# Kernel tuning notes

Hardware: AMD Instinct MI355X
Metric: run time of the kernel (lower is better)

The kernel has to match this reference:

```python
import jax, jax.numpy as jnp
import numpy as np

EPS = 1e-5  # BatchNorm2d default eps

def setup_inputs() -> dict:
    key = jax.random.key(0)
    k1, k2, k3, k4 = jax.random.split(key, 4)
    B, Cin, Cout, T, V = 64, 64, 128, 300, 25
    x = jax.random.normal(k1, (B, Cin, T, V), dtype=jnp.float32)
    adj = jax.random.uniform(k2, (V, V), dtype=jnp.float32)
    # Conv2d(kernel_size=1) weight (Cout, Cin), kaiming-ish scale
    W = jax.random.normal(k3, (Cout, Cin), dtype=jnp.float32) * (1.0 / np.sqrt(Cin))
    b = jnp.zeros((Cout,), dtype=jnp.float32)
    gamma = jnp.ones((Cout,), dtype=jnp.float32)
    beta = jnp.zeros((Cout,), dtype=jnp.float32)
    return {"x": x, "adj": adj, "W": W, "b": b, "gamma": gamma, "beta": beta}

def reference(x, adj, W, b, gamma, beta):
    # x: (B, C, T, V); graph aggregation over joints: matmul with adj on last dim
    xg = jnp.einsum('bctv,vw->bctw', x, adj)
    # 1x1 conv == per-(t,v) channel projection
    y = jnp.einsum('bctv,oc->botv', xg, W) + b[None, :, None, None]
    # BatchNorm2d (training mode): per-channel stats over (B, T, V), biased var
    mean = jnp.mean(y, axis=(0, 2, 3), keepdims=True)
    var = jnp.mean((y - mean) ** 2, axis=(0, 2, 3), keepdims=True)
    yn = (y - mean) * jax.lax.rsqrt(var + EPS)
    out = jax.nn.relu(gamma[None, :, None, None] * yn + beta[None, :, None, None])
    return out
```

## Files before the change

### kernel.cpp

```cpp
#include <hip/hip_runtime.h>
#include <hip/hip_bf16.h>
#include <stdint.h>

typedef __attribute__((ext_vector_type(8)))  short   short8;
typedef __attribute__((ext_vector_type(16))) float   floatx16;
typedef __attribute__((ext_vector_type(4)))  float   floatx4;

#define B_    64
#define CIN   64
#define COUT  128
#define T_    300
#define V_    25
#define NRED  (B_ * T_ * V_)
#define NSLOTS 32
#define NT    12
#define EPS   1e-5f

__device__ __forceinline__ uint32_t pk2(float a, float b) {
    union { __hip_bfloat162 h; uint32_t u; } c;
    c.h = __float22bfloat162_rn(make_float2(a, b));
    return c.u;
}

__device__ __forceinline__ floatx16 fzero16() {
    floatx16 z;
#pragma unroll
    for (int i = 0; i < 16; ++i) z[i] = 0.f;
    return z;
}

__device__ __forceinline__ int div25(int n) { return (n * 5243) >> 17; }

__device__ __forceinline__ void cvt_hb(const floatx16 h, int q, short8 hb[2]) {
    uint32_t pk[8], pp[8];
#pragma unroll
    for (int i = 0; i < 8; ++i) pk[i] = pk2(h[2 * i], h[2 * i + 1]);
#pragma unroll
    for (int i = 0; i < 8; ++i) pp[i] = (uint32_t)__shfl_xor((int)pk[i], 32, 64);
#pragma unroll
    for (int s = 0; s < 2; ++s) {
        union { short8 sv; uint32_t u[4]; } F;
        F.u[0] = q ? pp[4 * s + 2] : pk[4 * s];
        F.u[1] = q ? pp[4 * s + 3] : pk[4 * s + 1];
        F.u[2] = q ? pk[4 * s + 2] : pp[4 * s];
        F.u[3] = q ? pk[4 * s + 3] : pp[4 * s + 1];
        hb[s] = F.sv;
    }
}

__device__ __forceinline__ void build_const_frags(const float* __restrict__ W,
                                                  const float* __restrict__ adj,
                                                  int wave, int ln, int q,
                                                  short8 wf[4], short8 af[2]) {
    const float* wr = W + (32 * wave + ln) * CIN;
#pragma unroll
    for (int kk = 0; kk < 4; ++kk) {
        int c0 = 16 * kk + 8 * q;
        floatx4 a = *(const floatx4*)(wr + c0);
        floatx4 b = *(const floatx4*)(wr + c0 + 4);
        union { short8 sv; uint32_t u[4]; } F;
        F.u[0] = pk2(a[0], a[1]); F.u[1] = pk2(a[2], a[3]);
        F.u[2] = pk2(b[0], b[1]); F.u[3] = pk2(b[2], b[3]);
        wf[kk] = F.sv;
    }
#pragma unroll
    for (int s = 0; s < 2; ++s) {
        union { short8 sv; uint32_t u[4]; } F;
#pragma unroll
        for (int p = 0; p < 4; ++p) {
            int v0 = 16 * s + 8 * q + 2 * p;
            float e0 = (v0     < V_ && ln < V_) ? adj[v0 * V_ + ln]       : 0.f;
            float e1 = (v0 + 1 < V_ && ln < V_) ? adj[(v0 + 1) * V_ + ln] : 0.f;
            F.u[p] = pk2(e0, e1);
        }
        af[s] = F.sv;
    }
}

__device__ __forceinline__ void stage_x(const float* __restrict__ xb, int t4,
                                        float* __restrict__ ldsx, int tid) {
#pragma unroll
    for (int i = 0; i < 7; ++i) {
        int cid = i * 256 + tid;
        if (i < 6 || tid < 64) {
            int c  = div25(cid);
            int ch = cid - 25 * c;
            *(floatx4*)&ldsx[c * 100 + 4 * ch] =
                *(const floatx4*)(xb + c * 7500 + t4 * 25 + 4 * ch);
        }
    }
}

__device__ __forceinline__ void build_xa_lds(const float* __restrict__ ldsx,
                                             int tloc, int vcl, int q, short8 xa[4]) {
    const float* base = ldsx + tloc * 25 + vcl;
#pragma unroll
    for (int kk = 0; kk < 4; ++kk) {
        union { short8 sv; uint32_t u[4]; } F;
#pragma unroll
        for (int p = 0; p < 4; ++p) {
            int c0 = 16 * kk + 8 * q + 2 * p;
            F.u[p] = pk2(base[c0 * 100], base[(c0 + 1) * 100]);
        }
        xa[kk] = F.sv;
    }
}

__device__ __forceinline__ floatx16 compute_yt(const short8 xa[4], const short8 wf[4],
                                               const short8 af[2], int q) {
    floatx16 h = fzero16();
#pragma unroll
    for (int kk = 0; kk < 4; ++kk)
        h = __builtin_amdgcn_mfma_f32_32x32x16_bf16(xa[kk], wf[kk], h, 0, 0, 0);
    short8 hb[2];
    cvt_hb(h, q, hb);
    floatx16 y = fzero16();
#pragma unroll
    for (int s = 0; s < 2; ++s)
        y = __builtin_amdgcn_mfma_f32_32x32x16_bf16(af[s], hb[s], y, 0, 0, 0);
    return y;
}

__global__ __launch_bounds__(256, 3) void pass1_kernel(
    const float* __restrict__ x, const float* __restrict__ adj,
    const float* __restrict__ W,
    float* __restrict__ psum, float* __restrict__ psq)
{
    __shared__ __attribute__((aligned(16))) float ldsx[6400];

    const int tid  = threadIdx.x;
    const int wave = tid >> 6;
    const int lane = tid & 63;
    const int q    = lane >> 5;
    const int ln   = lane & 31;
    const int b    = blockIdx.y;
    const int tbase = blockIdx.x * NT;

    short8 wf[4], af[2];
    build_const_frags(W, adj, wave, ln, q, wf, af);
    const int vcl = ln < V_ ? ln : V_ - 1;
    const float* xb = x + (size_t)b * (CIN * T_ * V_);

    float sum = 0.f, sq = 0.f;
    for (int g = 0; g < NT / 4; ++g) {
        const int t4 = tbase + 4 * g;
        stage_x(xb, t4, ldsx, tid);
        __syncthreads();
#pragma unroll
        for (int tloc = 0; tloc < 4; ++tloc) {
            short8 xa[4];
            build_xa_lds(ldsx, tloc, vcl, q, xa);
            floatx16 y = compute_yt(xa, wf, af, q);
#pragma unroll
            for (int r = 0; r < 16; ++r) { sum += y[r]; sq += y[r] * y[r]; }
        }
        __syncthreads();
    }

    sum += __shfl_xor(sum, 32, 64);
    sq  += __shfl_xor(sq,  32, 64);
    if (q == 0) {
        int slot = (blockIdx.y * 25 + blockIdx.x) & (NSLOTS - 1);
        atomicAdd(&psum[slot * COUT + 32 * wave + ln], sum);
        atomicAdd(&psq [slot * COUT + 32 * wave + ln], sq);
    }
}

__global__ __launch_bounds__(256, 2) void pass2_kernel(
    const float* __restrict__ x, const float* __restrict__ adj,
    const float* __restrict__ W,
    const float* __restrict__ gamma, const float* __restrict__ beta,
    const float* __restrict__ psum, const float* __restrict__ psq,
    float* __restrict__ out)
{
    __shared__ __attribute__((aligned(16))) float ldsx[6400];
    __shared__ __attribute__((aligned(16))) float ldso[4][3200];

    const int tid  = threadIdx.x;
    const int wave = tid >> 6;
    const int lane = tid & 63;
    const int q    = lane >> 5;
    const int ln   = lane & 31;
    const int b    = blockIdx.y;
    const int tbase = blockIdx.x * NT;
    const int o_l  = 32 * wave + ln;

    short8 wf[4], af[2];
    build_const_frags(W, adj, wave, ln, q, wf, af);

    float s = 0.f, ss = 0.f;
#pragma unroll 4
    for (int k = 0; k < NSLOTS; ++k) {
        s  += psum[k * COUT + o_l];
        ss += psq [k * COUT + o_l];
    }
    const float mean = s / (float)NRED;
    const float var  = ss / (float)NRED - mean * mean;
    const float inv  = rsqrtf(var + EPS);
    const float sc   = gamma[o_l] * inv;
    const float sh   = beta[o_l] - mean * sc;

    const int vcl = ln < V_ ? ln : V_ - 1;
    const float* xb = x + (size_t)b * (CIN * T_ * V_);
    float* const ob = out + (size_t)(b * COUT + 32 * wave) * (T_ * V_);

    for (int g = 0; g < NT / 4; ++g) {
        const int t4 = tbase + 4 * g;
        stage_x(xb, t4, ldsx, tid);
        __syncthreads();

        float* const ow0 = &ldso[wave][ln * 100];
#pragma unroll
        for (int tloc = 0; tloc < 4; ++tloc) {
            short8 xa[4];
            build_xa_lds(ldsx, tloc, vcl, q, xa);
            floatx16 y = compute_yt(xa, wf, af, q);
            float* ow = ow0 + tloc * 25 + 4 * q;
#pragma unroll
            for (int g2 = 0; g2 < 3; ++g2) {
#pragma unroll
                for (int j = 0; j < 4; ++j) {
                    float v = sc * y[4 * g2 + j] + sh;
                    ow[8 * g2 + j] = v > 0.f ? v : 0.f;
                }
            }
            if (q == 0) {
                float v = sc * y[12] + sh;
                ow0[tloc * 25 + 24] = v > 0.f ? v : 0.f;
            }
        }

#pragma unroll
        for (int f = 0; f < 13; ++f) {
            int cid = f * 64 + lane;
            if (f < 12 || lane < 32) {
                int o = div25(cid);
                int c = cid - 25 * o;
                floatx4 v = *(const floatx4*)&ldso[wave][o * 100 + 4 * c];
                *(floatx4*)(ob + (size_t)o * (T_ * V_) + t4 * 25 + 4 * c) = v;
            }
        }
        __syncthreads();
    }
}


extern "C" void kernel_launch(void* const* d_in, const int* in_sizes, int n_in,
                              void* d_out, int out_size, void* d_ws, size_t ws_size,
                              hipStream_t stream) {
    const float* x     = (const float*)d_in[0];
    const float* adj   = (const float*)d_in[1];
    const float* W     = (const float*)d_in[2];
    const float* gamma = (const float*)d_in[4];
    const float* beta  = (const float*)d_in[5];
    float* out = (float*)d_out;

    float* psum = (float*)d_ws;
    float* psq  = (float*)((char*)d_ws + NSLOTS * COUT * sizeof(float));

    hipMemsetAsync(psum, 0, 2 * NSLOTS * COUT * sizeof(float), stream);

    dim3 grid(T_ / NT, B_);
    pass1_kernel<<<grid, 256, 0, stream>>>(x, adj, W, psum, psq);
    pass2_kernel<<<grid, 256, 0, stream>>>(x, adj, W, gamma, beta, psum, psq, out);
}
```

Baseline: 456.9 us.

## Compute transposed output tile and store directly, dropping LDS output staging

Pass 2 now computes the tile with output channels as rows and joints as columns (W-projection MFMA first, then adjacency MFMA), so each lane holds values for one joint across 16 channels. Results are written straight to global memory as scalar stores, removing the 50 KB LDS output buffer and its transpose/copy loop. Per-row BN scale and shift are gathered with lane shuffles, and launch bounds are raised to 3 blocks per SU to use the freed LDS. The trade-off is that the old 16-byte vector stores become scattered 4-byte stores with only 25 contiguous floats per row, and the changed launch bounds may increase register pressure.

```diff
diff --git a/kernel.cpp b/kernel.cpp
--- a/kernel.cpp
+++ b/kernel.cpp
@@ -166,7 +166,7 @@
     }
 }
 
-__global__ __launch_bounds__(256, 2) void pass2_kernel(
+__global__ __launch_bounds__(256, 3) void pass2_kernel(
     const float* __restrict__ x, const float* __restrict__ adj,
     const float* __restrict__ W,
     const float* __restrict__ gamma, const float* __restrict__ beta,
@@ -174,7 +174,6 @@
     float* __restrict__ out)
 {
     __shared__ __attribute__((aligned(16))) float ldsx[6400];
-    __shared__ __attribute__((aligned(16))) float ldso[4][3200];
 
     const int tid  = threadIdx.x;
     const int wave = tid >> 6;
@@ -188,56 +187,56 @@
     short8 wf[4], af[2];
     build_const_frags(W, adj, wave, ln, q, wf, af);
 
-    float s = 0.f, ss = 0.f;
+    float s0 = 0.f, ss = 0.f;
 #pragma unroll 4
     for (int k = 0; k < NSLOTS; ++k) {
-        s  += psum[k * COUT + o_l];
+        s0 += psum[k * COUT + o_l];
         ss += psq [k * COUT + o_l];
     }
-    const float mean = s / (float)NRED;
+    const float mean = s0 / (float)NRED;
     const float var  = ss / (float)NRED - mean * mean;
     const float inv  = rsqrtf(var + EPS);
-    const float sc   = gamma[o_l] * inv;
-    const float sh   = beta[o_l] - mean * sc;
+    const float sc0  = gamma[o_l] * inv;
+    const float sh0  = beta[o_l] - mean * sc0;
+
+    float scr[16], shr[16];
+#pragma unroll
+    for (int r = 0; r < 16; ++r) {
+        int src = (r & 3) + 8 * (r >> 2) + 4 * q;
+        scr[r] = __shfl(sc0, src, 64);
+        shr[r] = __shfl(sh0, src, 64);
+    }
 
     const int vcl = ln < V_ ? ln : V_ - 1;
     const float* xb = x + (size_t)b * (CIN * T_ * V_);
-    float* const ob = out + (size_t)(b * COUT + 32 * wave) * (T_ * V_);
+    float* const ob = out + (size_t)(b * COUT + 32 * wave + 4 * q) * (T_ * V_) + ln;
 
     for (int g = 0; g < NT / 4; ++g) {
         const int t4 = tbase + 4 * g;
         stage_x(xb, t4, ldsx, tid);
         __syncthreads();
-
-        float* const ow0 = &ldso[wave][ln * 100];
 #pragma unroll
         for (int tloc = 0; tloc < 4; ++tloc) {
             short8 xa[4];
             build_xa_lds(ldsx, tloc, vcl, q, xa);
-            floatx16 y = compute_yt(xa, wf, af, q);
-            float* ow = ow0 + tloc * 25 + 4 * q;
-#pragma unroll
-            for (int g2 = 0; g2 < 3; ++g2) {
-#pragma unroll
-                for (int j = 0; j < 4; ++j) {
-                    float v = sc * y[4 * g2 + j] + sh;
-                    ow[8 * g2 + j] = v > 0.f ? v : 0.f;
+            floatx16 h = fzero16();
+#pragma unroll
+            for (int kk = 0; kk < 4; ++kk)
+                h = __builtin_amdgcn_mfma_f32_32x32x16_bf16(xa[kk], wf[kk], h, 0, 0, 0);
+            short8 hb[2];
+            cvt_hb(h, q, hb);
+            floatx16 y = fzero16();
+#pragma unroll
+            for (int s2 = 0; s2 < 2; ++s2)
+                y = __builtin_amdgcn_mfma_f32_32x32x16_bf16(hb[s2], af[s2], y, 0, 0, 0);
+            if (ln < V_) {
+                float* pt = ob + (size_t)(t4 + tloc) * V_;
+#pragma unroll
+                for (int r = 0; r < 16; ++r) {
+                    const int orow = (r & 3) + 8 * (r >> 2);
+                    float v = scr[r] * y[r] + shr[r];
+                    pt[(size_t)orow * (T_ * V_)] = v > 0.f ? v : 0.f;
                 }
-            }
-            if (q == 0) {
-                float v = sc * y[12] + sh;
-                ow0[tloc * 25 + 24] = v > 0.f ? v : 0.f;
-            }
-        }
-
-#pragma unroll
-        for (int f = 0; f < 13; ++f) {
-            int cid = f * 64 + lane;
-            if (f < 12 || lane < 32) {
-                int o = div25(cid);
-                int c = cid - 25 * o;
-                floatx4 v = *(const floatx4*)&ldso[wave][o * 100 + 4 * c];
-                *(floatx4*)(ob + (size_t)o * (T_ * V_) + t4 * 25 + 4 * c) = v;
             }
         }
         __syncthreads();
```

New measurement: 472.1 us. 3.3% more time.

## Stage x tile as XOR-swizzled bf16 transposed layout in LDS

Applied to the files above, without the earlier changes.

The x tile staging now converts pairs of channels to packed bf16 at load time and stores them in a (t,v)-major LDS layout with an XOR swizzle. MFMA A-fragments can then be fetched with a single 128-bit LDS read per k-step instead of eight strided scalar reads plus per-use conversions. This halves the LDS footprint of the x tile and removes the bf16 conversion work repeated across the four waves. The cost is a scattered 32-bit store pattern during staging, and each global load now feeds one channel pair instead of a contiguous float4 row.

```diff
diff --git a/kernel.cpp b/kernel.cpp
--- a/kernel.cpp
+++ b/kernel.cpp
@@ -2,9 +2,10 @@
 #include <hip/hip_bf16.h>
 #include <stdint.h>
 
-typedef __attribute__((ext_vector_type(8)))  short   short8;
-typedef __attribute__((ext_vector_type(16))) float   floatx16;
-typedef __attribute__((ext_vector_type(4)))  float   floatx4;
+typedef __attribute__((ext_vector_type(8)))  short    short8;
+typedef __attribute__((ext_vector_type(16))) float    floatx16;
+typedef __attribute__((ext_vector_type(4)))  float    floatx4;
+typedef __attribute__((ext_vector_type(4)))  uint32_t uint4v;
 
 #define B_    64
 #define CIN   64
@@ -77,31 +78,37 @@
     }
 }
 
-__device__ __forceinline__ void stage_x(const float* __restrict__ xb, int t4,
-                                        float* __restrict__ ldsx, int tid) {
-#pragma unroll
-    for (int i = 0; i < 7; ++i) {
+__device__ __forceinline__ void stage_xT(const float* __restrict__ xb, int t4,
+                                         uint32_t* __restrict__ lds, int tid) {
+#pragma unroll
+    for (int i = 0; i < 4; ++i) {
         int cid = i * 256 + tid;
-        if (i < 6 || tid < 64) {
-            int c  = div25(cid);
-            int ch = cid - 25 * c;
-            *(floatx4*)&ldsx[c * 100 + 4 * ch] =
-                *(const floatx4*)(xb + c * 7500 + t4 * 25 + 4 * ch);
-        }
-    }
-}
-
-__device__ __forceinline__ void build_xa_lds(const float* __restrict__ ldsx,
-                                             int tloc, int vcl, int q, short8 xa[4]) {
-    const float* base = ldsx + tloc * 25 + vcl;
+        if (i < 3 || tid < 32) {
+            int ch = cid >> 5;
+            int cp = cid & 31;
+            const float* p0 = xb + (2 * cp) * 7500 + t4 * 25 + 4 * ch;
+            floatx4 a = *(const floatx4*)p0;
+            floatx4 b = *(const floatx4*)(p0 + 7500);
+            const int g  = cp >> 2;
+            const int c2 = cp & 3;
+#pragma unroll
+            for (int k = 0; k < 4; ++k) {
+                int tv = 4 * ch + k;
+                lds[tv * 32 + (((g ^ (tv & 7)) << 2) | c2)] = pk2(a[k], b[k]);
+            }
+        }
+    }
+}
+
+__device__ __forceinline__ void build_xa_ldsT(const uint32_t* __restrict__ lds,
+                                              int tloc, int vcl, int q, short8 xa[4]) {
+    const int tv = tloc * 25 + vcl;
+    const uint32_t* row = lds + tv * 32;
+    const int x7 = tv & 7;
 #pragma unroll
     for (int kk = 0; kk < 4; ++kk) {
-        union { short8 sv; uint32_t u[4]; } F;
-#pragma unroll
-        for (int p = 0; p < 4; ++p) {
-            int c0 = 16 * kk + 8 * q + 2 * p;
-            F.u[p] = pk2(base[c0 * 100], base[(c0 + 1) * 100]);
-        }
+        union { short8 sv; uint4v u4; } F;
+        F.u4 = *(const uint4v*)(row + (((q + 2 * kk) ^ x7) << 2));
         xa[kk] = F.sv;
     }
 }
@@ -126,7 +133,7 @@
     const float* __restrict__ W,
     float* __restrict__ psum, float* __restrict__ psq)
 {
-    __shared__ __attribute__((aligned(16))) float ldsx[6400];
+    __shared__ __attribute__((aligned(16))) uint32_t ldsx2[3200];
 
     const int tid  = threadIdx.x;
     const int wave = tid >> 6;
@@ -144,12 +151,12 @@
     float sum = 0.f, sq = 0.f;
     for (int g = 0; g < NT / 4; ++g) {
         const int t4 = tbase + 4 * g;
-        stage_x(xb, t4, ldsx, tid);
+        stage_xT(xb, t4, ldsx2, tid);
         __syncthreads();
 #pragma unroll
         for (int tloc = 0; tloc < 4; ++tloc) {
             short8 xa[4];
-            build_xa_lds(ldsx, tloc, vcl, q, xa);
+            build_xa_ldsT(ldsx2, tloc, vcl, q, xa);
             floatx16 y = compute_yt(xa, wf, af, q);
 #pragma unroll
             for (int r = 0; r < 16; ++r) { sum += y[r]; sq += y[r] * y[r]; }
@@ -173,7 +180,7 @@
     const float* __restrict__ psum, const float* __restrict__ psq,
     float* __restrict__ out)
 {
-    __shared__ __attribute__((aligned(16))) float ldsx[6400];
+    __shared__ __attribute__((aligned(16))) uint32_t ldsx2[3200];
     __shared__ __attribute__((aligned(16))) float ldso[4][3200];
 
     const int tid  = threadIdx.x;
@@ -206,14 +213,14 @@
 
     for (int g = 0; g < NT / 4; ++g) {
         const int t4 = tbase + 4 * g;
-        stage_x(xb, t4, ldsx, tid);
+        stage_xT(xb, t4, ldsx2, tid);
         __syncthreads();
 
         float* const ow0 = &ldso[wave][ln * 100];
 #pragma unroll
         for (int tloc = 0; tloc < 4; ++tloc) {
             short8 xa[4];
-            build_xa_lds(ldsx, tloc, vcl, q, xa);
+            build_xa_ldsT(ldsx2, tloc, vcl, q, xa);
             floatx16 y = compute_yt(xa, wf, af, q);
             float* ow = ow0 + tloc * 25 + 4 * q;
 #pragma unroll
```

Result: no change. 454.8 us (-0.5%).
